# Kernel optimization log

Hardware: AMD Instinct MI355X
Metric: run time of the kernel (lower is better)

## Reference

```python
import jax, jax.numpy as jnp
import numpy as np
from jax import lax

DEPTH = 8
N = 4_000_000
INIT_VEC = np.array([0.05, -0.1, 0.2, 0.0, 0.3, -0.2, 0.1, 0.05, -0.05], dtype=np.float32)


def setup_inputs() -> dict:
    key = jax.random.key(0)
    k_x, k_b = jax.random.split(key)
    x = jax.random.normal(k_x, (N, 9), dtype=jnp.float32)
    # Every layer's weight is initialized to the same init_vec (as in the torch module).
    weights = jnp.broadcast_to(jnp.asarray(INIT_VEC).reshape(1, 1, 1, 3, 3),
                               (DEPTH, 1, 1, 3, 3)).astype(jnp.float32)
    weights = jnp.array(weights)  # materialize per-layer copies (independent params)
    # Conv2d default bias init: U(-1/sqrt(fan_in), 1/sqrt(fan_in)), fan_in = 1*3*3 = 9.
    bound = 1.0 / 3.0
    biases = jax.random.uniform(k_b, (DEPTH,), minval=-bound, maxval=bound, dtype=jnp.float32)
    return {"input": x, "weights": weights, "biases": biases}


def reference(input, weights, biases):
    # input: [N, 9] -> [N, 1, 3, 3]
    h = input.reshape(-1, 1, 3, 3)
    depth = weights.shape[0]
    for d in range(depth):  # small fixed depth loop (structurally distinct params)
        h = lax.conv_general_dilated(
            h, weights[d],
            window_strides=(1, 1),
            padding=((1, 1), (1, 1)),
            dimension_numbers=("NCHW", "OIHW", "NCHW"),
        ) + biases[d]
    return h.reshape(-1, 9)
```

## Files before the change

### kernel.cpp

```cpp
#include <hip/hip_runtime.h>


typedef float v4f __attribute__((ext_vector_type(4)));

__global__ void compose_affine(const float* __restrict__ w,
                               const float* __restrict__ b,
                               float* __restrict__ aff)
{
    __shared__ float W[72];
    __shared__ float B[8];
    __shared__ float A[2][81];
    __shared__ float C[2][9];
    const int t = threadIdx.x;

    if (t < 72) W[t] = w[t];
    if (t >= 72 && t < 80) B[t - 72] = b[t - 72];
    if (t < 81) A[0][t] = (t / 9 == t % 9) ? 1.0f : 0.0f;
    if (t < 9)  C[0][t] = 0.0f;
    __syncthreads();

    int cur = 0;
    for (int d = 0; d < 8; ++d) {
        if (t < 81) {
            const int i = t / 9, j = t % 9;
            const int r = i / 3, cc = i % 3;
            float acc = 0.0f;
            float accc = (j == 0) ? B[d] : 0.0f;
            #pragma unroll
            for (int k = 0; k < 9; ++k) {
                const int rr = k / 3, kc = k % 3;
                const int dr = rr - r + 1, dc = kc - cc + 1;
                float m = 0.0f;
                if (dr >= 0 && dr < 3 && dc >= 0 && dc < 3)
                    m = W[d * 9 + dr * 3 + dc];
                acc = fmaf(m, A[cur][k * 9 + j], acc);
                if (j == 0) accc = fmaf(m, C[cur][k], accc);
            }
            A[1 - cur][t] = acc;
            if (j == 0) C[1 - cur][i] = accc;
        }
        __syncthreads();
        cur = 1 - cur;
    }
    if (t < 81) aff[t] = A[cur][t];
    if (t < 9)  aff[81 + t] = C[cur][t];
}

__global__ __launch_bounds__(64) void apply_affine(
    const v4f* __restrict__ in4,
    const float* __restrict__ aff,
    v4f* __restrict__ out4,
    long long n_f4)
{
    __shared__ float tile[2304];
    v4f* __restrict__ t4 = (v4f*)tile;
    const int L = threadIdx.x;
    const long long base = (long long)blockIdx.x * 576;

    v4f r[9];
    if (base + 576 <= n_f4) {
        #pragma unroll
        for (int j = 0; j < 9; ++j)
            r[j] = __builtin_nontemporal_load(in4 + base + L + (long long)j * 64);
    } else {
        #pragma unroll
        for (int j = 0; j < 9; ++j) {
            const long long g = base + L + (long long)j * 64;
            r[j] = (g < n_f4) ? __builtin_nontemporal_load(in4 + g) : (v4f)0.0f;
        }
    }
    #pragma unroll
    for (int j = 0; j < 9; ++j) t4[L + j * 64] = r[j];
    __syncthreads();

    #pragma unroll
    for (int jr = 0; jr < 4; ++jr) {
        const int row = L + jr * 64;
        float xv[9];
        #pragma unroll
        for (int j = 0; j < 9; ++j) xv[j] = tile[row * 9 + j];
        float y[9];
        #pragma unroll
        for (int i = 0; i < 9; ++i) y[i] = aff[81 + i];
        #pragma unroll
        for (int k = 0; k < 9; ++k) {
            #pragma unroll
            for (int i = 0; i < 9; ++i)
                y[i] = fmaf(aff[i * 9 + k], xv[k], y[i]);
        }
        #pragma unroll
        for (int j = 0; j < 9; ++j) tile[row * 9 + j] = y[j];
    }
    __syncthreads();

    #pragma unroll
    for (int j = 0; j < 9; ++j) r[j] = t4[L + j * 64];
    if (base + 576 <= n_f4) {
        #pragma unroll
        for (int j = 0; j < 9; ++j)
            __builtin_nontemporal_store(r[j], out4 + base + L + (long long)j * 64);
    } else {
        #pragma unroll
        for (int j = 0; j < 9; ++j) {
            const long long g = base + L + (long long)j * 64;
            if (g < n_f4) __builtin_nontemporal_store(r[j], out4 + g);
        }
    }
}

extern "C" void kernel_launch(void* const* d_in, const int* in_sizes, int n_in,
                              void* d_out, int out_size, void* d_ws, size_t ws_size,
                              hipStream_t stream) {
    const float* x = (const float*)d_in[0];
    const float* w = (const float*)d_in[1];
    const float* b = (const float*)d_in[2];
    float* out = (float*)d_out;
    float* aff = (float*)d_ws;

    const long long n_elems = (long long)in_sizes[0];
    const long long n_f4    = n_elems / 4;
    const long long tiles   = (n_f4 + 575) / 576;

    compose_affine<<<1, 128, 0, stream>>>(w, b, aff);
    apply_affine<<<dim3((unsigned)tiles), dim3(64), 0, stream>>>(
        (const v4f*)x, aff, (v4f*)out, n_f4);
}
```

Measured before the change: 245.9 us.

## Use persistent grid-stride blocks with register prefetch of the next tile

Turns the one-tile-per-block launch into a persistent grid of at most 4096 blocks that stride over tiles. Each block prefetches the next tile's input into registers while it computes and stores the current one, aiming to hide global load latency and cut block launch overhead. This adds an extra barrier per iteration and lowers the number of blocks, which can reduce memory-level parallelism for a bandwidth-bound kernel.

```diff
diff --git a/kernel.cpp b/kernel.cpp
--- a/kernel.cpp
+++ b/kernel.cpp
@@ -46,18 +46,11 @@
     if (t < 9)  aff[81 + t] = C[cur][t];
 }
 
-__global__ __launch_bounds__(64) void apply_affine(
-    const v4f* __restrict__ in4,
-    const float* __restrict__ aff,
-    v4f* __restrict__ out4,
-    long long n_f4)
+
+__device__ __forceinline__ void load_tile(v4f (&r)[9], const v4f* __restrict__ in4,
+                                          long long t, int L, long long n_f4)
 {
-    __shared__ float tile[2304];
-    v4f* __restrict__ t4 = (v4f*)tile;
-    const int L = threadIdx.x;
-    const long long base = (long long)blockIdx.x * 576;
-
-    v4f r[9];
+    const long long base = t * 576;
     if (base + 576 <= n_f4) {
         #pragma unroll
         for (int j = 0; j < 9; ++j)
@@ -69,42 +62,77 @@
             r[j] = (g < n_f4) ? __builtin_nontemporal_load(in4 + g) : (v4f)0.0f;
         }
     }
-    #pragma unroll
-    for (int j = 0; j < 9; ++j) t4[L + j * 64] = r[j];
-    __syncthreads();
+}
 
-    #pragma unroll
-    for (int jr = 0; jr < 4; ++jr) {
-        const int row = L + jr * 64;
-        float xv[9];
+__global__ __launch_bounds__(64) void apply_affine(
+    const v4f* __restrict__ in4,
+    const float* __restrict__ aff,
+    v4f* __restrict__ out4,
+    long long n_f4,
+    long long n_tiles)
+{
+    __shared__ float tile[2304];
+    v4f* __restrict__ t4 = (v4f*)tile;
+    const int L = threadIdx.x;
+    const long long stride = (long long)gridDim.x;
+
+    long long t = blockIdx.x;
+    if (t >= n_tiles) return;
+
+    v4f r[9];
+    load_tile(r, in4, t, L, n_f4);
+
+    for (;;) {
+        const long long base = t * 576;
+        const long long tn = t + stride;
+        const bool more = (tn < n_tiles);
+
         #pragma unroll
-        for (int j = 0; j < 9; ++j) xv[j] = tile[row * 9 + j];
-        float y[9];
+        for (int j = 0; j < 9; ++j) t4[L + j * 64] = r[j];
+        __syncthreads();
+
+        if (more) load_tile(r, in4, tn, L, n_f4);
+
         #pragma unroll
-        for (int i = 0; i < 9; ++i) y[i] = aff[81 + i];
-        #pragma unroll
-        for (int k = 0; k < 9; ++k) {
+        for (int jr = 0; jr < 4; ++jr) {
+            const int row = L + jr * 64;
+            float xv[9];
             #pragma unroll
-            for (int i = 0; i < 9; ++i)
-                y[i] = fmaf(aff[i * 9 + k], xv[k], y[i]);
+            for (int j = 0; j < 9; ++j) xv[j] = tile[row * 9 + j];
+            float y[9];
+            #pragma unroll
+            for (int i = 0; i < 9; ++i) y[i] = aff[81 + i];
+            #pragma unroll
+            for (int k = 0; k < 9; ++k) {
+                #pragma unroll
+                for (int i = 0; i < 9; ++i)
+                    y[i] = fmaf(aff[i * 9 + k], xv[k], y[i]);
+            }
+            #pragma unroll
+            for (int j = 0; j < 9; ++j) tile[row * 9 + j] = y[j];
         }
-        #pragma unroll
-        for (int j = 0; j < 9; ++j) tile[row * 9 + j] = y[j];
-    }
-    __syncthreads();
+        __syncthreads();
 
-    #pragma unroll
-    for (int j = 0; j < 9; ++j) r[j] = t4[L + j * 64];
-    if (base + 576 <= n_f4) {
-        #pragma unroll
-        for (int j = 0; j < 9; ++j)
-            __builtin_nontemporal_store(r[j], out4 + base + L + (long long)j * 64);
-    } else {
-        #pragma unroll
-        for (int j = 0; j < 9; ++j) {
-            const long long g = base + L + (long long)j * 64;
-            if (g < n_f4) __builtin_nontemporal_store(r[j], out4 + g);
+        if (base + 576 <= n_f4) {
+            #pragma unroll
+            for (int j = 0; j < 9; ++j) {
+                const v4f o = t4[L + j * 64];
+                __builtin_nontemporal_store(o, out4 + base + L + (long long)j * 64);
+            }
+        } else {
+            #pragma unroll
+            for (int j = 0; j < 9; ++j) {
+                const long long g = base + L + (long long)j * 64;
+                if (g < n_f4) {
+                    const v4f o = t4[L + j * 64];
+                    __builtin_nontemporal_store(o, out4 + g);
+                }
+            }
         }
+
+        if (!more) break;
+        t = tn;
+        __syncthreads();
     }
 }
 
@@ -121,7 +149,10 @@
     const long long n_f4    = n_elems / 4;
     const long long tiles   = (n_f4 + 575) / 576;
 
+    const long long max_blocks = 4096;
+    const unsigned blocks = (unsigned)((tiles < max_blocks) ? tiles : max_blocks);
+
     compose_affine<<<1, 128, 0, stream>>>(w, b, aff);
-    apply_affine<<<dim3((unsigned)tiles), dim3(64), 0, stream>>>(
-        (const v4f*)x, aff, (v4f*)out, n_f4);
+    apply_affine<<<dim3(blocks), dim3(64), 0, stream>>>(
+        (const v4f*)x, aff, (v4f*)out, n_f4, tiles);
 }
```

Result: no change. 250.1 us (+1.7%).

## Process four rows per thread from registers instead of an LDS-staged tile

Applied to the files above, without the earlier changes.

Each thread now loads nine contiguous float4s (four 9-float rows) straight into registers, applies the composed affine map there and writes them back, which removes the shared-memory tile, both barriers and the nontemporal hints. Blocks grow from 64 to 256 threads, and leftover rows are handled by one extra thread. The cost is uncoalesced access: neighbouring lanes are 144 bytes apart, so each wave's vector loads span many cache lines per instruction, and register pressure rises.

```diff
diff --git a/kernel.cpp b/kernel.cpp
--- a/kernel.cpp
+++ b/kernel.cpp
@@ -46,64 +46,61 @@
     if (t < 9)  aff[81 + t] = C[cur][t];
 }
 
-__global__ __launch_bounds__(64) void apply_affine(
+__global__ __launch_bounds__(256) void apply_affine_rows(
     const v4f* __restrict__ in4,
     const float* __restrict__ aff,
     v4f* __restrict__ out4,
-    long long n_f4)
+    long long n_groups,
+    long long rem_rows)
 {
-    __shared__ float tile[2304];
-    v4f* __restrict__ t4 = (v4f*)tile;
-    const int L = threadIdx.x;
-    const long long base = (long long)blockIdx.x * 576;
+    const long long g = (long long)blockIdx.x * blockDim.x + threadIdx.x;
 
-    v4f r[9];
-    if (base + 576 <= n_f4) {
+    if (g < n_groups) {
+        const v4f* __restrict__ ip = in4 + g * 9;
+        v4f d[9];
         #pragma unroll
-        for (int j = 0; j < 9; ++j)
-            r[j] = __builtin_nontemporal_load(in4 + base + L + (long long)j * 64);
-    } else {
+        for (int j = 0; j < 9; ++j) d[j] = ip[j];
+
         #pragma unroll
-        for (int j = 0; j < 9; ++j) {
-            const long long g = base + L + (long long)j * 64;
-            r[j] = (g < n_f4) ? __builtin_nontemporal_load(in4 + g) : (v4f)0.0f;
+        for (int r = 0; r < 4; ++r) {
+            float xv[9];
+            #pragma unroll
+            for (int k = 0; k < 9; ++k) {
+                const int fi = 9 * r + k;
+                xv[k] = d[fi >> 2][fi & 3];
+            }
+            float y[9];
+            #pragma unroll
+            for (int i = 0; i < 9; ++i) y[i] = aff[81 + i];
+            #pragma unroll
+            for (int k = 0; k < 9; ++k) {
+                #pragma unroll
+                for (int i = 0; i < 9; ++i)
+                    y[i] = fmaf(aff[i * 9 + k], xv[k], y[i]);
+            }
+            #pragma unroll
+            for (int k = 0; k < 9; ++k) {
+                const int fi = 9 * r + k;
+                d[fi >> 2][fi & 3] = y[k];
+            }
         }
-    }
-    #pragma unroll
-    for (int j = 0; j < 9; ++j) t4[L + j * 64] = r[j];
-    __syncthreads();
 
-    #pragma unroll
-    for (int jr = 0; jr < 4; ++jr) {
-        const int row = L + jr * 64;
-        float xv[9];
+        v4f* __restrict__ op = out4 + g * 9;
         #pragma unroll
-        for (int j = 0; j < 9; ++j) xv[j] = tile[row * 9 + j];
-        float y[9];
-        #pragma unroll
-        for (int i = 0; i < 9; ++i) y[i] = aff[81 + i];
-        #pragma unroll
-        for (int k = 0; k < 9; ++k) {
-            #pragma unroll
-            for (int i = 0; i < 9; ++i)
-                y[i] = fmaf(aff[i * 9 + k], xv[k], y[i]);
-        }
-        #pragma unroll
-        for (int j = 0; j < 9; ++j) tile[row * 9 + j] = y[j];
-    }
-    __syncthreads();
-
-    #pragma unroll
-    for (int j = 0; j < 9; ++j) r[j] = t4[L + j * 64];
-    if (base + 576 <= n_f4) {
-        #pragma unroll
-        for (int j = 0; j < 9; ++j)
-            __builtin_nontemporal_store(r[j], out4 + base + L + (long long)j * 64);
-    } else {
-        #pragma unroll
-        for (int j = 0; j < 9; ++j) {
-            const long long g = base + L + (long long)j * 64;
-            if (g < n_f4) __builtin_nontemporal_store(r[j], out4 + g);
+        for (int j = 0; j < 9; ++j) op[j] = d[j];
+    } else if (g == n_groups && rem_rows > 0) {
+        const float* __restrict__ inf = (const float*)in4;
+        float* __restrict__ outf = (float*)out4;
+        for (int r = 0; r < (int)rem_rows; ++r) {
+            const long long base = (n_groups * 4 + r) * 9;
+            float xv[9];
+            for (int k = 0; k < 9; ++k) xv[k] = inf[base + k];
+            float y[9];
+            for (int i = 0; i < 9; ++i) y[i] = aff[81 + i];
+            for (int k = 0; k < 9; ++k)
+                for (int i = 0; i < 9; ++i)
+                    y[i] = fmaf(aff[i * 9 + k], xv[k], y[i]);
+            for (int k = 0; k < 9; ++k) outf[base + k] = y[k];
         }
     }
 }
@@ -117,11 +114,15 @@
     float* out = (float*)d_out;
     float* aff = (float*)d_ws;
 
-    const long long n_elems = (long long)in_sizes[0];
-    const long long n_f4    = n_elems / 4;
-    const long long tiles   = (n_f4 + 575) / 576;
+    const long long n_elems  = (long long)in_sizes[0];
+    const long long n_rows   = n_elems / 9;
+    const long long n_groups = n_rows / 4;
+    const long long rem_rows = n_rows % 4;
+
+    const long long n_threads = n_groups + (rem_rows ? 1 : 0);
+    const unsigned blocks = (unsigned)((n_threads + 255) / 256);
 
     compose_affine<<<1, 128, 0, stream>>>(w, b, aff);
-    apply_affine<<<dim3((unsigned)tiles), dim3(64), 0, stream>>>(
-        (const v4f*)x, aff, (v4f*)out, n_f4);
+    apply_affine_rows<<<dim3(blocks), dim3(256), 0, stream>>>(
+        (const v4f*)x, aff, (v4f*)out, n_groups, rem_rows);
 }
```

Result: slower. 280.4 us (+14.0%).
